# Optimization experiments

Measured on AMD Instinct MI355X. Metric: run time of the kernel, lower is better.

Reference implementation:

```python
import jax, jax.numpy as jnp
import numpy as np

N_NODES = 100000
N_EDGES = 1600000
F_IN = 128
F_OUT = 128


def _spmm(edge_row, edge_col, edge_weight, X):
    # sparse [N,N] @ dense [N,F]: gather source rows, weight, scatter-add to dest rows
    msgs = edge_weight[:, None] * X[edge_col]  # [E, F]
    return jax.ops.segment_sum(msgs, edge_row, num_segments=N_NODES)


def setup_inputs() -> dict:
    key = jax.random.key(0)
    ks = jax.random.split(key, 7)
    scale = 1.0 / np.sqrt(F_IN)
    return {
        "x": jax.random.normal(ks[0], (N_NODES, F_IN), dtype=jnp.float32),
        "edge_row": jax.random.randint(ks[1], (N_EDGES,), 0, N_NODES, dtype=jnp.int32),
        "edge_col": jax.random.randint(ks[2], (N_EDGES,), 0, N_NODES, dtype=jnp.int32),
        "edge_weight": jax.random.uniform(ks[3], (N_EDGES,), dtype=jnp.float32),
        "w1": jax.random.normal(ks[4], (F_IN, F_IN), dtype=jnp.float32) * scale,
        "w2": jax.random.normal(ks[5], (F_IN, F_OUT), dtype=jnp.float32) * scale,
        "w3": jax.random.normal(ks[6], (F_OUT, F_OUT), dtype=jnp.float32) * scale,
    }


def reference(x, edge_row, edge_col, edge_weight, w1, w2, w3):
    # dropout p=0.0 (eval) -> identity
    h = jax.nn.relu(_spmm(edge_row, edge_col, edge_weight, x @ w1))
    h = jax.nn.relu(_spmm(edge_row, edge_col, edge_weight, h @ w2))
    h = jax.nn.relu(_spmm(edge_row, edge_col, edge_weight, h @ w3))
    return h
```

## Files before the change

kernel.cpp:

```cpp
#include <hip/hip_runtime.h>

#define N_NODES 100000
#define N_EDGES 1600000
#define F 128

#define SCAN_B 1024
#define SCAN_NB ((N_NODES + SCAN_B - 1) / SCAN_B)

#define NSHARD 8
#define SHARD_E (N_EDGES / NSHARD)

#define NCHUNK 128
#define CHUNK_E (N_EDGES / NCHUNK)
#define HALF_N 50000

typedef short bf16x8 __attribute__((ext_vector_type(8)));
typedef float f32x4  __attribute__((ext_vector_type(4)));

union ABFrag {
    bf16x8 v;
    unsigned short u[8];
    uint4  q;
};

__device__ __forceinline__ unsigned short f2bf(float f) {
    unsigned int u = __float_as_uint(f);
    u += 0x7fffu + ((u >> 16) & 1u);
    return (unsigned short)(u >> 16);
}
__device__ __forceinline__ float bflo(unsigned int u) {
    return __uint_as_float(u << 16);
}
__device__ __forceinline__ float bfhi(unsigned int u) {
    return __uint_as_float(u & 0xFFFF0000u);
}


__global__ __launch_bounds__(256) void chunk_hist(
    const int* __restrict__ erow, unsigned char* __restrict__ counts8) {
    __shared__ unsigned int h[HALF_N / 4];
    const int c = blockIdx.x;
    const int t = threadIdx.x;
#pragma unroll
    for (int half = 0; half < 2; ++half) {
        for (int i = t; i < HALF_N / 4; i += 256) h[i] = 0;
        __syncthreads();
        const int lo = half * HALF_N;
        for (int e = c * CHUNK_E + t; e < (c + 1) * CHUNK_E; e += 256) {
            const unsigned int d = (unsigned int)(erow[e] - lo);
            if (d < HALF_N) atomicAdd(&h[d >> 2], 1u << ((d & 3u) * 8u));
        }
        __syncthreads();
        unsigned int* dw = (unsigned int*)(counts8 + (size_t)c * N_NODES + lo);
        for (int i = t; i < HALF_N / 4; i += 256) dw[i] = h[i];
        __syncthreads();
    }
}

__global__ __launch_bounds__(256) void chunk_prefix(
    const unsigned char* __restrict__ counts8,
    unsigned char* __restrict__ base8, int* __restrict__ counts) {
    const int w = blockIdx.x * 256 + threadIdx.x;
    if (w >= N_NODES / 4) return;
    unsigned int run = 0;
    for (int c = 0; c < NCHUNK; ++c) {
        ((unsigned int*)(base8 + (size_t)c * N_NODES))[w] = run;
        run += ((const unsigned int*)(counts8 + (size_t)c * N_NODES))[w];
    }
    const int n = w * 4;
    counts[n + 0] = run & 255u;
    counts[n + 1] = (run >> 8) & 255u;
    counts[n + 2] = (run >> 16) & 255u;
    counts[n + 3] = run >> 24;
}

__global__ void scan_block_sums(const int* __restrict__ counts, int* __restrict__ bsums) {
    __shared__ int s[SCAN_B];
    const int t = threadIdx.x;
    const int idx = blockIdx.x * SCAN_B + t;
    int v = (idx < N_NODES) ? counts[idx] : 0;
    s[t] = v;
    __syncthreads();
    for (int off = SCAN_B / 2; off > 0; off >>= 1) {
        if (t < off) s[t] += s[t + off];
        __syncthreads();
    }
    if (t == 0) bsums[blockIdx.x] = s[0];
}

__global__ void scan_bsums(const int* __restrict__ bsums, int* __restrict__ boffs) {
    __shared__ int s[128];
    const int t = threadIdx.x;
    int v = (t < SCAN_NB) ? bsums[t] : 0;
    s[t] = v;
    __syncthreads();
    for (int off = 1; off < 128; off <<= 1) {
        int u = (t >= off) ? s[t - off] : 0;
        __syncthreads();
        s[t] += u;
        __syncthreads();
    }
    if (t < SCAN_NB) boffs[t] = s[t] - v;
}

__global__ void scan_final(const int* __restrict__ counts, const int* __restrict__ boffs,
                           int* __restrict__ row_ptr) {
    __shared__ int s[SCAN_B];
    const int t = threadIdx.x;
    const int idx = blockIdx.x * SCAN_B + t;
    int v = (idx < N_NODES) ? counts[idx] : 0;
    s[t] = v;
    __syncthreads();
    for (int off = 1; off < SCAN_B; off <<= 1) {
        int u = (t >= off) ? s[t - off] : 0;
        __syncthreads();
        s[t] += u;
        __syncthreads();
    }
    if (idx < N_NODES) row_ptr[idx] = boffs[blockIdx.x] + s[t] - v;
    if (idx == 0) row_ptr[N_NODES] = N_EDGES;
}

__global__ __launch_bounds__(256) void chunk_rank(
    const int* __restrict__ erow, const int* __restrict__ ecol,
    const float* __restrict__ ew,
    const unsigned char* __restrict__ base8, const int* __restrict__ row_ptr,
    unsigned long long* __restrict__ rec) {
    __shared__ unsigned int h[HALF_N / 4];
    const int c = blockIdx.x;
    const int t = threadIdx.x;
#pragma unroll
    for (int half = 0; half < 2; ++half) {
        for (int i = t; i < HALF_N / 4; i += 256) h[i] = 0;
        __syncthreads();
        const int lo = half * HALF_N;
        for (int e = c * CHUNK_E + t; e < (c + 1) * CHUNK_E; e += 256) {
            const int dst = erow[e];
            const unsigned int d = (unsigned int)(dst - lo);
            if (d < HALF_N) {
                const unsigned int old = atomicAdd(&h[d >> 2], 1u << ((d & 3u) * 8u));
                const unsigned int lrank = (old >> ((d & 3u) * 8u)) & 255u;
                const unsigned int pos = (unsigned int)row_ptr[dst]
                                       + (unsigned int)base8[(size_t)c * N_NODES + dst]
                                       + lrank;
                const unsigned int colw = ((unsigned int)ecol[e] << 15)
                                        | (unsigned int)f2bf(ew[e]);
                rec[e] = ((unsigned long long)pos << 32) | colw;
            }
        }
        __syncthreads();
    }
}

__global__ __launch_bounds__(256) void csr_fill_sharded(
    const unsigned long long* __restrict__ rec,
    unsigned int* __restrict__ pairs) {
    const int shard = blockIdx.x & (NSHARD - 1);
    const int e = (blockIdx.x >> 3) * 256 + threadIdx.x;
    const unsigned long long v = rec[e];
    const unsigned int pos = (unsigned int)(v >> 32);
    if ((unsigned int)(pos - (unsigned int)(shard * SHARD_E)) < (unsigned int)SHARD_E) {
        pairs[pos] = (unsigned int)v;
    }
}

__global__ void transpose_w_bf16(const float* __restrict__ W, unsigned short* __restrict__ Wt) {
    const int i = blockIdx.x * 256 + threadIdx.x;
    const int n = i >> 7;
    const int k = i & 127;
    Wt[i] = f2bf(W[k * F + n]);
}

__global__ __launch_bounds__(256) void gemm_mfma(
    const float* __restrict__ Xf,
    const unsigned short* __restrict__ Xb,
    const unsigned short* __restrict__ Wt,
    unsigned short* __restrict__ Y,
    int use_f32_in)
{
    __shared__ unsigned short Wl[4 * 8 * 64 * 8];

    const int tid  = threadIdx.x;
    const int wave = tid >> 6;
    const int lane = tid & 63;

    for (int s = tid; s < 2048; s += 256) {
        const int ln  = s & 63;
        const int ntk = s >> 6;
        const int nt  = ntk & 7;
        const int kt  = ntk >> 3;
        const int n   = nt * 16 + (ln & 15);
        const int k   = kt * 32 + (ln >> 4) * 8;
        *(uint4*)(&Wl[s * 8]) = *(const uint4*)(Wt + n * F + k);
    }
    __syncthreads();

    const int m     = blockIdx.x * 64 + wave * 16 + (lane & 15);
    const bool mval = (m < N_NODES);
    const int kq    = (lane >> 4) * 8;

    f32x4 acc[8] = {};

#pragma unroll
    for (int kt = 0; kt < 4; ++kt) {
        ABFrag a;
        if (mval) {
            if (use_f32_in) {
                const float* p = Xf + (size_t)m * F + kt * 32 + kq;
                const float4 u0 = *(const float4*)p;
                const float4 u1 = *(const float4*)(p + 4);
                a.u[0] = f2bf(u0.x); a.u[1] = f2bf(u0.y);
                a.u[2] = f2bf(u0.z); a.u[3] = f2bf(u0.w);
                a.u[4] = f2bf(u1.x); a.u[5] = f2bf(u1.y);
                a.u[6] = f2bf(u1.z); a.u[7] = f2bf(u1.w);
            } else {
                a.q = *(const uint4*)(Xb + (size_t)m * F + kt * 32 + kq);
#pragma unroll
                for (int j = 0; j < 8; ++j)
                    if (a.u[j] & 0x8000u) a.u[j] = 0;
            }
        } else {
            a.q = make_uint4(0, 0, 0, 0);
        }
#pragma unroll
        for (int nt = 0; nt < 8; ++nt) {
            ABFrag b;
            b.q = *(const uint4*)(&Wl[((kt * 8 + nt) * 64 + lane) * 8]);
            acc[nt] = __builtin_amdgcn_mfma_f32_16x16x32_bf16(a.v, b.v, acc[nt], 0, 0, 0);
        }
    }

    const int rbase = blockIdx.x * 64 + wave * 16 + (lane >> 4) * 4;
    const int cbase = lane & 15;
#pragma unroll
    for (int r = 0; r < 4; ++r) {
        const int row = rbase + r;
        if (row < N_NODES) {
#pragma unroll
            for (int nt = 0; nt < 8; ++nt) {
                Y[(size_t)row * F + nt * 16 + cbase] = f2bf(acc[nt][r]);
            }
        }
    }
}

__global__ __launch_bounds__(256) void spmm_csr_bf16(
    const unsigned short* __restrict__ Xb,
    const int* __restrict__ row_ptr,
    const unsigned int* __restrict__ pairs,
    unsigned short* __restrict__ Ob,
    float* __restrict__ Of,
    int final_mode) {
    const int tid = threadIdx.x;
    const int l16 = tid & 15;
    const int q   = tid >> 4;
    const int row = blockIdx.x * 16 + q;

    const int beg = row_ptr[row];
    const int end = row_ptr[row + 1];

    float a[8] = {};
    int i = beg;
    for (; i + 1 < end; i += 2) {
        const unsigned int p0 = pairs[i], p1 = pairs[i + 1];
        const uint4 v0 = *(const uint4*)(Xb + (size_t)(p0 >> 15) * F + l16 * 8);
        const uint4 v1 = *(const uint4*)(Xb + (size_t)(p1 >> 15) * F + l16 * 8);
        const float w0 = bflo(p0 & 0x7FFFu);
        const float w1 = bflo(p1 & 0x7FFFu);
        a[0] += w0 * bflo(v0.x); a[1] += w0 * bfhi(v0.x);
        a[2] += w0 * bflo(v0.y); a[3] += w0 * bfhi(v0.y);
        a[4] += w0 * bflo(v0.z); a[5] += w0 * bfhi(v0.z);
        a[6] += w0 * bflo(v0.w); a[7] += w0 * bfhi(v0.w);
        a[0] += w1 * bflo(v1.x); a[1] += w1 * bfhi(v1.x);
        a[2] += w1 * bflo(v1.y); a[3] += w1 * bfhi(v1.y);
        a[4] += w1 * bflo(v1.z); a[5] += w1 * bfhi(v1.z);
        a[6] += w1 * bflo(v1.w); a[7] += w1 * bfhi(v1.w);
    }
    if (i < end) {
        const unsigned int p0 = pairs[i];
        const uint4 v0 = *(const uint4*)(Xb + (size_t)(p0 >> 15) * F + l16 * 8);
        const float w0 = bflo(p0 & 0x7FFFu);
        a[0] += w0 * bflo(v0.x); a[1] += w0 * bfhi(v0.x);
        a[2] += w0 * bflo(v0.y); a[3] += w0 * bfhi(v0.y);
        a[4] += w0 * bflo(v0.z); a[5] += w0 * bfhi(v0.z);
        a[6] += w0 * bflo(v0.w); a[7] += w0 * bfhi(v0.w);
    }

    if (final_mode) {
        float4 o0 = {fmaxf(a[0], 0.f), fmaxf(a[1], 0.f), fmaxf(a[2], 0.f), fmaxf(a[3], 0.f)};
        float4 o1 = {fmaxf(a[4], 0.f), fmaxf(a[5], 0.f), fmaxf(a[6], 0.f), fmaxf(a[7], 0.f)};
        float* p = Of + (size_t)row * F + l16 * 8;
        *(float4*)p = o0;
        *(float4*)(p + 4) = o1;
    } else {
        uint4 o;
        o.x = (unsigned int)f2bf(a[0]) | ((unsigned int)f2bf(a[1]) << 16);
        o.y = (unsigned int)f2bf(a[2]) | ((unsigned int)f2bf(a[3]) << 16);
        o.z = (unsigned int)f2bf(a[4]) | ((unsigned int)f2bf(a[5]) << 16);
        o.w = (unsigned int)f2bf(a[6]) | ((unsigned int)f2bf(a[7]) << 16);
        *(uint4*)(Ob + (size_t)row * F + l16 * 8) = o;
    }
}


extern "C" void kernel_launch(void* const* d_in, const int* in_sizes, int n_in,
                              void* d_out, int out_size, void* d_ws, size_t ws_size,
                              hipStream_t stream) {
    const float* x    = (const float*)d_in[0];
    const int*   erow = (const int*)d_in[1];
    const int*   ecol = (const int*)d_in[2];
    const float* ew   = (const float*)d_in[3];
    const float* w1   = (const float*)d_in[4];
    const float* w2   = (const float*)d_in[5];
    const float* w3   = (const float*)d_in[6];
    float* out = (float*)d_out;

    char* ws = (char*)d_ws;
    size_t off = 0;
    auto alloc = [&](size_t bytes) -> char* {
        char* p = ws + off;
        off += (bytes + 255) & ~(size_t)255;
        return p;
    };
    unsigned short* bufA = (unsigned short*)alloc((size_t)N_NODES * F * 2);
    unsigned short* bufB = (unsigned short*)alloc((size_t)N_NODES * F * 2);
    unsigned int* pairs  = (unsigned int*)alloc((size_t)N_EDGES * 4);
    int* counts  = (int*)alloc((size_t)N_NODES * sizeof(int));
    int* row_ptr = (int*)alloc(((size_t)N_NODES + 1) * sizeof(int));
    int* bsums   = (int*)alloc((size_t)SCAN_NB * sizeof(int));
    int* boffs   = (int*)alloc((size_t)SCAN_NB * sizeof(int));
    unsigned short* wt1 = (unsigned short*)alloc((size_t)F * F * 2);
    unsigned short* wt2 = (unsigned short*)alloc((size_t)F * F * 2);
    unsigned short* wt3 = (unsigned short*)alloc((size_t)F * F * 2);

    unsigned char* counts8 = (unsigned char*)bufA;
    unsigned char* base8   = (unsigned char*)bufA + (size_t)NCHUNK * N_NODES;
    unsigned long long* rec = (unsigned long long*)bufB;

    chunk_hist<<<NCHUNK, 256, 0, stream>>>(erow, counts8);
    chunk_prefix<<<(N_NODES / 4 + 255) / 256, 256, 0, stream>>>(counts8, base8, counts);
    scan_block_sums<<<SCAN_NB, SCAN_B, 0, stream>>>(counts, bsums);
    scan_bsums<<<1, 128, 0, stream>>>(bsums, boffs);
    scan_final<<<SCAN_NB, SCAN_B, 0, stream>>>(counts, boffs, row_ptr);
    chunk_rank<<<NCHUNK, 256, 0, stream>>>(erow, ecol, ew, base8, row_ptr, rec);
    csr_fill_sharded<<<(N_EDGES / 256) * NSHARD, 256, 0, stream>>>(rec, pairs);

    transpose_w_bf16<<<64, 256, 0, stream>>>(w1, wt1);
    transpose_w_bf16<<<64, 256, 0, stream>>>(w2, wt2);
    transpose_w_bf16<<<64, 256, 0, stream>>>(w3, wt3);

    const int ggrid = (N_NODES + 63) / 64;
    const int sgrid = N_NODES / 16;

    gemm_mfma<<<ggrid, 256, 0, stream>>>(x, nullptr, wt1, bufA, 1);
    spmm_csr_bf16<<<sgrid, 256, 0, stream>>>(bufA, row_ptr, pairs, bufB, nullptr, 0);
    gemm_mfma<<<ggrid, 256, 0, stream>>>(nullptr, bufB, wt2, bufA, 0);
    spmm_csr_bf16<<<sgrid, 256, 0, stream>>>(bufA, row_ptr, pairs, bufB, nullptr, 0);
    gemm_mfma<<<ggrid, 256, 0, stream>>>(nullptr, bufB, wt3, bufA, 0);
    spmm_csr_bf16<<<sgrid, 256, 0, stream>>>(bufA, row_ptr, pairs, nullptr, out, 1);
}
```

Before: 494.9 us.

## Parallelize CSR build preprocessing across more chunks, halves, and prefix lanes

Doubles the number of edge chunks and splits each chunk's two node halves into separate blocks for the histogram and rank kernels, so 512 blocks run instead of 128. The per-node chunk prefix is split across 8 lanes with a shuffle scan and is done in place, removing the separate base buffer. The aim is to fill the GPU during the CSR build, which previously used few blocks. In exchange each block rereads the full chunk of edge rows and there is more chunk-count traffic. The byte-packed counts also now depend on smaller chunks staying under 256 edges per node.

```diff
diff --git a/kernel.cpp b/kernel.cpp
--- a/kernel.cpp
+++ b/kernel.cpp
@@ -10,7 +10,7 @@
 #define NSHARD 8
 #define SHARD_E (N_EDGES / NSHARD)
 
-#define NCHUNK 128
+#define NCHUNK 256
 #define CHUNK_E (N_EDGES / NCHUNK)
 #define HALF_N 50000
 
@@ -37,41 +37,57 @@
 
 
 __global__ __launch_bounds__(256) void chunk_hist(
-    const int* __restrict__ erow, unsigned char* __restrict__ counts8) {
+    const int* __restrict__ erow, unsigned char* __restrict__ cb) {
     __shared__ unsigned int h[HALF_N / 4];
-    const int c = blockIdx.x;
-    const int t = threadIdx.x;
-#pragma unroll
-    for (int half = 0; half < 2; ++half) {
-        for (int i = t; i < HALF_N / 4; i += 256) h[i] = 0;
-        __syncthreads();
-        const int lo = half * HALF_N;
-        for (int e = c * CHUNK_E + t; e < (c + 1) * CHUNK_E; e += 256) {
-            const unsigned int d = (unsigned int)(erow[e] - lo);
-            if (d < HALF_N) atomicAdd(&h[d >> 2], 1u << ((d & 3u) * 8u));
-        }
-        __syncthreads();
-        unsigned int* dw = (unsigned int*)(counts8 + (size_t)c * N_NODES + lo);
-        for (int i = t; i < HALF_N / 4; i += 256) dw[i] = h[i];
-        __syncthreads();
-    }
+    const int c    = blockIdx.x >> 1;
+    const int half = blockIdx.x & 1;
+    const int t    = threadIdx.x;
+    for (int i = t; i < HALF_N / 4; i += 256) h[i] = 0;
+    __syncthreads();
+    const int lo = half * HALF_N;
+    for (int e = c * CHUNK_E + t; e < (c + 1) * CHUNK_E; e += 256) {
+        const unsigned int d = (unsigned int)(erow[e] - lo);
+        if (d < HALF_N) atomicAdd(&h[d >> 2], 1u << ((d & 3u) * 8u));
+    }
+    __syncthreads();
+    unsigned int* dw = (unsigned int*)(cb + (size_t)c * N_NODES + lo);
+    for (int i = t; i < HALF_N / 4; i += 256) dw[i] = h[i];
 }
 
 __global__ __launch_bounds__(256) void chunk_prefix(
-    const unsigned char* __restrict__ counts8,
-    unsigned char* __restrict__ base8, int* __restrict__ counts) {
-    const int w = blockIdx.x * 256 + threadIdx.x;
-    if (w >= N_NODES / 4) return;
-    unsigned int run = 0;
-    for (int c = 0; c < NCHUNK; ++c) {
-        ((unsigned int*)(base8 + (size_t)c * N_NODES))[w] = run;
-        run += ((const unsigned int*)(counts8 + (size_t)c * N_NODES))[w];
-    }
-    const int n = w * 4;
-    counts[n + 0] = run & 255u;
-    counts[n + 1] = (run >> 8) & 255u;
-    counts[n + 2] = (run >> 16) & 255u;
-    counts[n + 3] = run >> 24;
+    unsigned char* __restrict__ cb, int* __restrict__ counts) {
+    const int t = blockIdx.x * 256 + threadIdx.x;
+    if (t >= (N_NODES / 4) * 8) return;
+    const int w   = t >> 3;
+    const int sub = t & 7;
+    const int c0  = sub * (NCHUNK / 8);
+    unsigned int v[NCHUNK / 8];
+    unsigned int sum = 0;
+#pragma unroll
+    for (int j = 0; j < NCHUNK / 8; ++j) {
+        v[j] = *(const unsigned int*)(cb + (size_t)(c0 + j) * N_NODES + 4 * (size_t)w);
+        sum += v[j];
+    }
+    unsigned int run = sum;
+#pragma unroll
+    for (int d = 1; d < 8; d <<= 1) {
+        unsigned int tmp = __shfl_up(run, d, 8);
+        if (sub >= d) run += tmp;
+    }
+    unsigned int acc = run - sum;
+#pragma unroll
+    for (int j = 0; j < NCHUNK / 8; ++j) {
+        const unsigned int old = v[j];
+        *(unsigned int*)(cb + (size_t)(c0 + j) * N_NODES + 4 * (size_t)w) = acc;
+        acc += old;
+    }
+    if (sub == 7) {
+        const int n = w * 4;
+        counts[n + 0] = run & 255u;
+        counts[n + 1] = (run >> 8) & 255u;
+        counts[n + 2] = (run >> 16) & 255u;
+        counts[n + 3] = run >> 24;
+    }
 }
 
 __global__ void scan_block_sums(const int* __restrict__ counts, int* __restrict__ bsums) {
@@ -124,31 +140,28 @@
 __global__ __launch_bounds__(256) void chunk_rank(
     const int* __restrict__ erow, const int* __restrict__ ecol,
     const float* __restrict__ ew,
-    const unsigned char* __restrict__ base8, const int* __restrict__ row_ptr,
+    const unsigned char* __restrict__ cb, const int* __restrict__ row_ptr,
     unsigned long long* __restrict__ rec) {
     __shared__ unsigned int h[HALF_N / 4];
-    const int c = blockIdx.x;
-    const int t = threadIdx.x;
-#pragma unroll
-    for (int half = 0; half < 2; ++half) {
-        for (int i = t; i < HALF_N / 4; i += 256) h[i] = 0;
-        __syncthreads();
-        const int lo = half * HALF_N;
-        for (int e = c * CHUNK_E + t; e < (c + 1) * CHUNK_E; e += 256) {
-            const int dst = erow[e];
-            const unsigned int d = (unsigned int)(dst - lo);
-            if (d < HALF_N) {
-                const unsigned int old = atomicAdd(&h[d >> 2], 1u << ((d & 3u) * 8u));
-                const unsigned int lrank = (old >> ((d & 3u) * 8u)) & 255u;
-                const unsigned int pos = (unsigned int)row_ptr[dst]
-                                       + (unsigned int)base8[(size_t)c * N_NODES + dst]
-                                       + lrank;
-                const unsigned int colw = ((unsigned int)ecol[e] << 15)
-                                        | (unsigned int)f2bf(ew[e]);
-                rec[e] = ((unsigned long long)pos << 32) | colw;
-            }
+    const int c    = blockIdx.x >> 1;
+    const int half = blockIdx.x & 1;
+    const int t    = threadIdx.x;
+    for (int i = t; i < HALF_N / 4; i += 256) h[i] = 0;
+    __syncthreads();
+    const int lo = half * HALF_N;
+    for (int e = c * CHUNK_E + t; e < (c + 1) * CHUNK_E; e += 256) {
+        const int dst = erow[e];
+        const unsigned int d = (unsigned int)(dst - lo);
+        if (d < HALF_N) {
+            const unsigned int old = atomicAdd(&h[d >> 2], 1u << ((d & 3u) * 8u));
+            const unsigned int lrank = (old >> ((d & 3u) * 8u)) & 255u;
+            const unsigned int pos = (unsigned int)row_ptr[dst]
+                                   + (unsigned int)cb[(size_t)c * N_NODES + dst]
+                                   + lrank;
+            const unsigned int colw = ((unsigned int)ecol[e] << 15)
+                                    | (unsigned int)f2bf(ew[e]);
+            rec[e] = ((unsigned long long)pos << 32) | colw;
         }
-        __syncthreads();
     }
 }
 
@@ -333,16 +346,15 @@
     unsigned short* wt2 = (unsigned short*)alloc((size_t)F * F * 2);
     unsigned short* wt3 = (unsigned short*)alloc((size_t)F * F * 2);
 
-    unsigned char* counts8 = (unsigned char*)bufA;
-    unsigned char* base8   = (unsigned char*)bufA + (size_t)NCHUNK * N_NODES;
+    unsigned char* cb = (unsigned char*)bufA;
     unsigned long long* rec = (unsigned long long*)bufB;
 
-    chunk_hist<<<NCHUNK, 256, 0, stream>>>(erow, counts8);
-    chunk_prefix<<<(N_NODES / 4 + 255) / 256, 256, 0, stream>>>(counts8, base8, counts);
+    chunk_hist<<<NCHUNK * 2, 256, 0, stream>>>(erow, cb);
+    chunk_prefix<<<((N_NODES / 4) * 8 + 255) / 256, 256, 0, stream>>>(cb, counts);
     scan_block_sums<<<SCAN_NB, SCAN_B, 0, stream>>>(counts, bsums);
     scan_bsums<<<1, 128, 0, stream>>>(bsums, boffs);
     scan_final<<<SCAN_NB, SCAN_B, 0, stream>>>(counts, boffs, row_ptr);
-    chunk_rank<<<NCHUNK, 256, 0, stream>>>(erow, ecol, ew, base8, row_ptr, rec);
+    chunk_rank<<<NCHUNK * 2, 256, 0, stream>>>(erow, ecol, ew, cb, row_ptr, rec);
     csr_fill_sharded<<<(N_EDGES / 256) * NSHARD, 256, 0, stream>>>(rec, pairs);
 
     transpose_w_bf16<<<64, 256, 0, stream>>>(w1, wt1);
```

New measurement: 449.5 us. 9.2% less time.
